# Optimization experiments

Hardware: AMD Instinct MI355X
Metric: run time of the kernel (lower is better)

The kernel has to match this reference:

```python
import jax, jax.numpy as jnp
import numpy as np

# Plane axes from generate_planes(); projection uses their inverses (permutation matrices).
_PLANES = np.array([[[1, 0, 0], [0, 1, 0], [0, 0, 1]],
                    [[1, 0, 0], [0, 0, 1], [0, 1, 0]],
                    [[0, 0, 1], [1, 0, 0], [0, 1, 0]]], dtype=np.float32)
_INV_PLANES = np.linalg.inv(_PLANES)  # [3,3,3]


def _grid_sample_2d(feat, grid):
    """Bilinear grid_sample, padding_mode='zeros', align_corners=False.
    feat: [C,H,W], grid: [M,2] with (x,y) in normalized coords. Returns [C,M]."""
    C, H, W = feat.shape
    x = ((grid[:, 0] + 1.0) * W - 1.0) * 0.5  # [M] pixel coords
    y = ((grid[:, 1] + 1.0) * H - 1.0) * 0.5
    x0 = jnp.floor(x)
    y0 = jnp.floor(y)
    wx = x - x0  # weight of right/bottom neighbor
    wy = y - y0
    x0i = x0.astype(jnp.int32)
    y0i = y0.astype(jnp.int32)
    x1i = x0i + 1
    y1i = y0i + 1

    def corner(xi, yi):
        valid = (xi >= 0) & (xi < W) & (yi >= 0) & (yi < H)
        xc = jnp.clip(xi, 0, W - 1)
        yc = jnp.clip(yi, 0, H - 1)
        v = feat[:, yc, xc]  # [C, M] gather
        return v * valid.astype(feat.dtype)

    v00 = corner(x0i, y0i)
    v10 = corner(x1i, y0i)
    v01 = corner(x0i, y1i)
    v11 = corner(x1i, y1i)
    out = (v00 * (1.0 - wx) * (1.0 - wy)
           + v10 * wx * (1.0 - wy)
           + v01 * (1.0 - wx) * wy
           + v11 * wx * wy)
    return out  # [C, M]


def setup_inputs() -> dict:
    key = jax.random.key(0)
    k1, k2, k3 = jax.random.split(key, 3)
    N, P, C, H, W, M = 4, 3, 32, 256, 256, 500000
    planes = jax.random.normal(k1, (N, P, C, H, W), dtype=jnp.float32)
    sample_coordinates = jax.random.uniform(k2, (N, M, 3), dtype=jnp.float32,
                                            minval=-1.0, maxval=1.0)
    sample_directions = jax.random.normal(k3, (N, M, 3), dtype=jnp.float32)
    return {"planes": planes, "sample_coordinates": sample_coordinates,
            "sample_directions": sample_directions}


def reference(planes, sample_coordinates, sample_directions):
    # ImportanceRenderer.run_model: project -> grid_sample per plane -> mean over planes.
    N, n_planes, C, H, W = planes.shape
    M = sample_coordinates.shape[1]
    inv = jnp.asarray(_INV_PLANES, dtype=sample_coordinates.dtype)  # [P,3,3]
    # torch.bmm(coords, inv_planes): [N,P,M,3] @ [P,3,3] -> take first 2 dims
    proj = jnp.einsum('nmi,pij->npmj', sample_coordinates, inv)[..., :2]  # [N,P,M,2]
    feats = planes.reshape(N * n_planes, C, H, W)
    grids = proj.reshape(N * n_planes, M, 2)
    sampled = jax.vmap(_grid_sample_2d)(feats, grids)  # [N*P, C, M]
    sampled = sampled.reshape(N, n_planes, C, M).transpose(0, 1, 3, 2)  # [N,P,M,C]
    return sampled.mean(axis=1)  # [N, M, C]
```

## Files before the change

kernel.cpp:

```cpp
#include <hip/hip_runtime.h>
#include <hip/hip_fp16.h>


constexpr int Cc = 32, Hh = 256, Ww = 256, Pp = 3, Nn = 4;
constexpr int HWPIX = Hh * Ww;
constexpr int NCO   = 4096;
constexpr int CB    = 2048;

__device__ inline unsigned spread3(unsigned x) {
    x &= 0x3FFu;
    x = (x | (x << 16)) & 0x030000FFu;
    x = (x | (x << 8))  & 0x0300F00Fu;
    x = (x | (x << 4))  & 0x030C30C3u;
    x = (x | (x << 2))  & 0x09249249u;
    return x;
}
__device__ inline unsigned coarse_key(float cx, float cy, float cz) {
    const int a = min(max((int)((cx + 1.0f) * 8.0f), 0), 15);
    const int b = min(max((int)((cy + 1.0f) * 8.0f), 0), 15);
    const int c = min(max((int)((cz + 1.0f) * 8.0f), 0), 15);
    return spread3((unsigned)a) | (spread3((unsigned)b) << 1) | (spread3((unsigned)c) << 2);
}

__global__ __launch_bounds__(256) void transpose_chw_hwc_h(
    const float* __restrict__ in, __half* __restrict__ out)
{
    __shared__ float lds[Cc * 257];
    const int slice = blockIdx.y;
    const int pix0  = blockIdx.x * 256;
    const int t     = threadIdx.x;

    const float* src = in + (size_t)slice * Cc * HWPIX + pix0 + t;
    #pragma unroll
    for (int c = 0; c < Cc; ++c)
        lds[c * 257 + t] = src[(size_t)c * HWPIX];
    __syncthreads();

    uint4* dst = reinterpret_cast<uint4*>(
        out + (size_t)slice * HWPIX * Cc + (size_t)pix0 * Cc);
    #pragma unroll
    for (int k = 0; k < 4; ++k) {
        const int idx = k * 256 + t;
        const int pix = idx >> 2;
        const int c0  = (idx & 3) * 8;
        unsigned r[4];
        #pragma unroll
        for (int j = 0; j < 4; ++j) {
            const __half h0 = __float2half(lds[(c0 + 2 * j + 0) * 257 + pix]);
            const __half h1 = __float2half(lds[(c0 + 2 * j + 1) * 257 + pix]);
            r[j] = (unsigned)__half_as_ushort(h0)
                 | ((unsigned)__half_as_ushort(h1) << 16);
        }
        dst[idx] = make_uint4(r[0], r[1], r[2], r[3]);
    }
}

__global__ __launch_bounds__(256) void block_hist(
    const float* __restrict__ coords, unsigned* __restrict__ bh, int M, int nb)
{
    __shared__ unsigned h[NCO];
    const int n = blockIdx.y, b = blockIdx.x, t = threadIdx.x;
    #pragma unroll
    for (int k = 0; k < NCO / 256; ++k) h[k * 256 + t] = 0u;
    __syncthreads();

    const int base = b * CB;
    for (int j = t; j < CB; j += 256) {
        const int m = base + j;
        if (m < M) {
            const float* cp = coords + ((size_t)n * M + m) * 3;
            atomicAdd(&h[coarse_key(cp[0], cp[1], cp[2])], 1u);
        }
    }
    __syncthreads();
    unsigned* dst = bh + ((size_t)n * nb + b) * NCO;
    #pragma unroll
    for (int k = 0; k < NCO / 256; ++k) dst[k * 256 + t] = h[k * 256 + t];
}

__global__ __launch_bounds__(256) void col_prefix(
    unsigned* __restrict__ bh, unsigned* __restrict__ tot, int nb)
{
    const int n = blockIdx.y;
    const int c = blockIdx.x * 256 + threadIdx.x;
    unsigned* p = bh + (size_t)n * nb * NCO + c;
    unsigned run = 0;
    for (int b = 0; b < nb; ++b) {
        const unsigned v = p[(size_t)b * NCO];
        p[(size_t)b * NCO] = run;
        run += v;
    }
    tot[n * NCO + c] = run;
}

__global__ __launch_bounds__(1024) void cell_scan(unsigned* __restrict__ tot)
{
    __shared__ unsigned lds[1024];
    unsigned* h = tot + (size_t)blockIdx.x * NCO;
    const int t = threadIdx.x;
    unsigned v[4];
    unsigned s = 0;
    #pragma unroll
    for (int i = 0; i < 4; ++i) { v[i] = h[t * 4 + i]; s += v[i]; }
    lds[t] = s;
    __syncthreads();
    for (int d = 1; d < 1024; d <<= 1) {
        const unsigned add = (t >= d) ? lds[t - d] : 0u;
        __syncthreads();
        lds[t] += add;
        __syncthreads();
    }
    unsigned base = (t > 0) ? lds[t - 1] : 0u;
    #pragma unroll
    for (int i = 0; i < 4; ++i) { const unsigned tmp = v[i]; h[t * 4 + i] = base; base += tmp; }
}

__global__ __launch_bounds__(256) void block_scatter(
    const float* __restrict__ coords, const unsigned* __restrict__ bh,
    const unsigned* __restrict__ cellbase, unsigned* __restrict__ idx,
    int M, int nb)
{
    __shared__ unsigned h[NCO];
    const int n = blockIdx.y, b = blockIdx.x, t = threadIdx.x;
    #pragma unroll
    for (int k = 0; k < NCO / 256; ++k) h[k * 256 + t] = 0u;
    __syncthreads();

    const unsigned* myrow = bh + ((size_t)n * nb + b) * NCO;
    const int base = b * CB;
    for (int j = t; j < CB; j += 256) {
        const int m = base + j;
        if (m < M) {
            const float* cp = coords + ((size_t)n * M + m) * 3;
            const unsigned k = coarse_key(cp[0], cp[1], cp[2]);
            const unsigned r = atomicAdd(&h[k], 1u);
            const unsigned slot = cellbase[n * NCO + k] + myrow[k] + r;
            idx[(size_t)n * M + slot] = (unsigned)m;
        }
    }
}

__global__ __launch_bounds__(256) void triplane_gather4h(
    const __half* __restrict__ tp, const unsigned* __restrict__ idx,
    const float* __restrict__ coords, float* __restrict__ out,
    int M, int gx, int nwg)
{
    int bid = blockIdx.x;
    {
        const int q = nwg >> 3, r = nwg & 7;
        const int xcd = bid & 7, i = bid >> 3;
        bid = (xcd < r ? xcd * (q + 1) : r * (q + 1) + (xcd - r) * q) + i;
    }
    const int n  = bid / gx;
    const int bx = bid - n * gx;
    const int gid  = bx * 256 + threadIdx.x;
    const int s    = gid >> 2;
    const int quad = gid & 3;
    if (s >= M) return;

    const int m = (int)idx[(size_t)n * M + s];
    const float* cp = coords + ((size_t)n * M + m) * 3;
    const float cx = cp[0], cy = cp[1], cz = cp[2];

    const uint4* addr[12];
    __half2 wh[12];

    #pragma unroll
    for (int p = 0; p < 3; ++p) {
        const float gxc = (p == 2) ? cz : cx;
        const float gyc = (p == 0) ? cy : ((p == 1) ? cz : cx);
        const float x = ((gxc + 1.0f) * 256.0f - 1.0f) * 0.5f;
        const float y = ((gyc + 1.0f) * 256.0f - 1.0f) * 0.5f;
        const float x0f = floorf(x), y0f = floorf(y);
        const float wx = x - x0f, wy = y - y0f;
        const int x0 = (int)x0f, y0 = (int)y0f;
        const int x1 = x0 + 1,   y1 = y0 + 1;
        const bool vx0 = (unsigned)x0 < 256u;
        const bool vx1 = (unsigned)x1 < 256u;
        const bool vy0 = (unsigned)y0 < 256u;
        const bool vy1 = (unsigned)y1 < 256u;
        const int cx0 = min(max(x0, 0), 255), cx1 = min(max(x1, 0), 255);
        const int cy0 = min(max(y0, 0), 255), cy1 = min(max(y1, 0), 255);

        const float w00 = ((vx0 && vy0) ? 1.f : 0.f) * (1.f - wx) * (1.f - wy);
        const float w10 = ((vx1 && vy0) ? 1.f : 0.f) * wx * (1.f - wy);
        const float w01 = ((vx0 && vy1) ? 1.f : 0.f) * (1.f - wx) * wy;
        const float w11 = ((vx1 && vy1) ? 1.f : 0.f) * wx * wy;
        wh[p * 4 + 0] = __float2half2_rn(w00);
        wh[p * 4 + 1] = __float2half2_rn(w10);
        wh[p * 4 + 2] = __float2half2_rn(w01);
        wh[p * 4 + 3] = __float2half2_rn(w11);

        const uint4* base = reinterpret_cast<const uint4*>(
            tp + (size_t)(n * 3 + p) * HWPIX * Cc);
        addr[p * 4 + 0] = base + (size_t)((cy0 << 8) + cx0) * 4 + quad;
        addr[p * 4 + 1] = base + (size_t)((cy0 << 8) + cx1) * 4 + quad;
        addr[p * 4 + 2] = base + (size_t)((cy1 << 8) + cx0) * 4 + quad;
        addr[p * 4 + 3] = base + (size_t)((cy1 << 8) + cx1) * 4 + quad;
    }

    uint4 rv[12];
    #pragma unroll
    for (int j = 0; j < 12; ++j) rv[j] = *addr[j];

    float accx[8];
    #pragma unroll
    for (int i = 0; i < 8; ++i) accx[i] = 0.f;

    #pragma unroll
    for (int p = 0; p < 3; ++p) {
        __half2 a0 = __float2half2_rn(0.f), a1 = a0, a2 = a0, a3 = a0;
        #pragma unroll
        for (int c = 0; c < 4; ++c) {
            const uint4 v = rv[p * 4 + c];
            const __half2 w = wh[p * 4 + c];
            a0 = __hfma2(*reinterpret_cast<const __half2*>(&v.x), w, a0);
            a1 = __hfma2(*reinterpret_cast<const __half2*>(&v.y), w, a1);
            a2 = __hfma2(*reinterpret_cast<const __half2*>(&v.z), w, a2);
            a3 = __hfma2(*reinterpret_cast<const __half2*>(&v.w), w, a3);
        }
        const float2 f0 = __half22float2(a0);
        const float2 f1 = __half22float2(a1);
        const float2 f2 = __half22float2(a2);
        const float2 f3 = __half22float2(a3);
        accx[0] += f0.x; accx[1] += f0.y;
        accx[2] += f1.x; accx[3] += f1.y;
        accx[4] += f2.x; accx[5] += f2.y;
        accx[6] += f3.x; accx[7] += f3.y;
    }

    constexpr float third = 1.0f / 3.0f;
    float4 o0, o1;
    o0.x = accx[0] * third; o0.y = accx[1] * third;
    o0.z = accx[2] * third; o0.w = accx[3] * third;
    o1.x = accx[4] * third; o1.y = accx[5] * third;
    o1.z = accx[6] * third; o1.w = accx[7] * third;

    float4* op = reinterpret_cast<float4*>(out + ((size_t)n * M + m) * Cc);
    op[quad * 2 + 0] = o0;
    op[quad * 2 + 1] = o1;
}

__global__ __launch_bounds__(256) void triplane_gather_hwc8h(
    const __half* __restrict__ tp, const float* __restrict__ coords,
    float* __restrict__ out, int M)
{
    const int gid   = blockIdx.x * 256 + threadIdx.x;
    const int m     = gid >> 3;
    const int chunk = gid & 7;
    const int n     = blockIdx.y;
    if (m >= M) return;

    const float* cp = coords + ((size_t)n * M + m) * 3;
    const float cx = cp[0], cy = cp[1], cz = cp[2];

    const uint2* addr[12];
    float w[12];

    #pragma unroll
    for (int p = 0; p < 3; ++p) {
        const float gxc = (p == 2) ? cz : cx;
        const float gyc = (p == 0) ? cy : ((p == 1) ? cz : cx);
        const float x = ((gxc + 1.0f) * 256.0f - 1.0f) * 0.5f;
        const float y = ((gyc + 1.0f) * 256.0f - 1.0f) * 0.5f;
        const float x0f = floorf(x), y0f = floorf(y);
        const float wx = x - x0f, wy = y - y0f;
        const int x0 = (int)x0f, y0 = (int)y0f;
        const int x1 = x0 + 1,   y1 = y0 + 1;
        const bool vx0 = (unsigned)x0 < 256u;
        const bool vx1 = (unsigned)x1 < 256u;
        const bool vy0 = (unsigned)y0 < 256u;
        const bool vy1 = (unsigned)y1 < 256u;
        const int cx0 = min(max(x0, 0), 255), cx1 = min(max(x1, 0), 255);
        const int cy0 = min(max(y0, 0), 255), cy1 = min(max(y1, 0), 255);

        w[p * 4 + 0] = ((vx0 && vy0) ? 1.f : 0.f) * (1.f - wx) * (1.f - wy);
        w[p * 4 + 1] = ((vx1 && vy0) ? 1.f : 0.f) * wx * (1.f - wy);
        w[p * 4 + 2] = ((vx0 && vy1) ? 1.f : 0.f) * (1.f - wx) * wy;
        w[p * 4 + 3] = ((vx1 && vy1) ? 1.f : 0.f) * wx * wy;

        const uint2* base = reinterpret_cast<const uint2*>(
            tp + (size_t)(n * 3 + p) * HWPIX * Cc);
        addr[p * 4 + 0] = base + (size_t)((cy0 << 8) + cx0) * 8 + chunk;
        addr[p * 4 + 1] = base + (size_t)((cy0 << 8) + cx1) * 8 + chunk;
        addr[p * 4 + 2] = base + (size_t)((cy1 << 8) + cx0) * 8 + chunk;
        addr[p * 4 + 3] = base + (size_t)((cy1 << 8) + cx1) * 8 + chunk;
    }

    uint2 rv[12];
    #pragma unroll
    for (int j = 0; j < 12; ++j) rv[j] = *addr[j];

    float4 acc = make_float4(0.f, 0.f, 0.f, 0.f);
    #pragma unroll
    for (int j = 0; j < 12; ++j) {
        const __half2 h0 = *reinterpret_cast<const __half2*>(&rv[j].x);
        const __half2 h1 = *reinterpret_cast<const __half2*>(&rv[j].y);
        const float2 f0 = __half22float2(h0);
        const float2 f1 = __half22float2(h1);
        acc.x += w[j] * f0.x;
        acc.y += w[j] * f0.y;
        acc.z += w[j] * f1.x;
        acc.w += w[j] * f1.y;
    }

    constexpr float third = 1.0f / 3.0f;
    acc.x *= third; acc.y *= third; acc.z *= third; acc.w *= third;

    float4* op = reinterpret_cast<float4*>(out + ((size_t)n * M + m) * Cc);
    op[chunk] = acc;
}

__global__ __launch_bounds__(256) void triplane_gather_chw(
    const float* __restrict__ planes, const float* __restrict__ coords,
    float* __restrict__ out, int M)
{
    const int m = blockIdx.x * 256 + threadIdx.x;
    const int n = blockIdx.y;
    if (m >= M) return;

    const float* cp = coords + ((size_t)n * M + m) * 3;
    const float cx = cp[0], cy = cp[1], cz = cp[2];

    int   off[3][4];
    float w[3][4];
    #pragma unroll
    for (int p = 0; p < 3; ++p) {
        const float gxc = (p == 2) ? cz : cx;
        const float gyc = (p == 0) ? cy : ((p == 1) ? cz : cx);
        const float x = ((gxc + 1.0f) * 256.0f - 1.0f) * 0.5f;
        const float y = ((gyc + 1.0f) * 256.0f - 1.0f) * 0.5f;
        const float x0f = floorf(x), y0f = floorf(y);
        const float wx = x - x0f, wy = y - y0f;
        const int x0 = (int)x0f, y0 = (int)y0f;
        const int x1 = x0 + 1,   y1 = y0 + 1;
        const bool vx0 = (unsigned)x0 < 256u, vx1 = (unsigned)x1 < 256u;
        const bool vy0 = (unsigned)y0 < 256u, vy1 = (unsigned)y1 < 256u;
        const int cx0 = min(max(x0, 0), 255), cx1 = min(max(x1, 0), 255);
        const int cy0 = min(max(y0, 0), 255), cy1 = min(max(y1, 0), 255);
        off[p][0] = (cy0 << 8) + cx0;  w[p][0] = ((vx0 && vy0) ? 1.f : 0.f) * (1.f - wx) * (1.f - wy);
        off[p][1] = (cy0 << 8) + cx1;  w[p][1] = ((vx1 && vy0) ? 1.f : 0.f) * wx * (1.f - wy);
        off[p][2] = (cy1 << 8) + cx0;  w[p][2] = ((vx0 && vy1) ? 1.f : 0.f) * (1.f - wx) * wy;
        off[p][3] = (cy1 << 8) + cx1;  w[p][3] = ((vx1 && vy1) ? 1.f : 0.f) * wx * wy;
    }

    float* op = out + ((size_t)n * M + m) * Cc;
    constexpr float third = 1.0f / 3.0f;
    for (int c = 0; c < Cc; ++c) {
        float a = 0.f;
        #pragma unroll
        for (int p = 0; p < 3; ++p) {
            const float* b = planes + ((size_t)(n * 3 + p) * Cc + c) * HWPIX;
            a += w[p][0] * b[off[p][0]] + w[p][1] * b[off[p][1]]
               + w[p][2] * b[off[p][2]] + w[p][3] * b[off[p][3]];
        }
        op[c] = a * third;
    }
}

extern "C" void kernel_launch(void* const* d_in, const int* in_sizes, int n_in,
                              void* d_out, int out_size, void* d_ws, size_t ws_size,
                              hipStream_t stream)
{
    const float* planes = (const float*)d_in[0];
    const float* coords = (const float*)d_in[1];
    float* out = (float*)d_out;

    const int M  = in_sizes[1] / (Nn * 3);
    const int nb = (M + CB - 1) / CB;

    auto align256 = [](size_t x) { return (x + 255) & ~(size_t)255; };
    const size_t tph_bytes = align256((size_t)Nn * Pp * HWPIX * Cc * sizeof(__half));
    const size_t idx_bytes = align256((size_t)Nn * M * sizeof(unsigned));
    const size_t bh_bytes  = align256((size_t)Nn * nb * NCO * sizeof(unsigned));
    const size_t tot_bytes = align256((size_t)Nn * NCO * sizeof(unsigned));

    if (ws_size >= tph_bytes + idx_bytes + bh_bytes + tot_bytes) {
        char* p = (char*)d_ws;
        __half*   tp  = (__half*)p;    p += tph_bytes;
        unsigned* idx = (unsigned*)p;  p += idx_bytes;
        unsigned* bh  = (unsigned*)p;  p += bh_bytes;
        unsigned* tot = (unsigned*)p;

        transpose_chw_hwc_h<<<dim3(HWPIX / 256, Nn * Pp), 256, 0, stream>>>(planes, tp);
        block_hist<<<dim3(nb, Nn), 256, 0, stream>>>(coords, bh, M, nb);
        col_prefix<<<dim3(NCO / 256, Nn), 256, 0, stream>>>(bh, tot, nb);
        cell_scan<<<Nn, 1024, 0, stream>>>(tot);
        block_scatter<<<dim3(nb, Nn), 256, 0, stream>>>(coords, bh, tot, idx, M, nb);

        const int gx  = (M * 4 + 255) / 256;
        const int nwg = Nn * gx;
        triplane_gather4h<<<nwg, 256, 0, stream>>>(tp, idx, coords, out, M, gx, nwg);
    } else if (ws_size >= tph_bytes) {
        __half* tp = (__half*)d_ws;
        transpose_chw_hwc_h<<<dim3(HWPIX / 256, Nn * Pp), 256, 0, stream>>>(planes, tp);
        const int gx = (M * 8 + 255) / 256;
        triplane_gather_hwc8h<<<dim3(gx, Nn), 256, 0, stream>>>(tp, coords, out, M);
    } else {
        const int gx = (M + 255) / 256;
        triplane_gather_chw<<<dim3(gx, Nn), 256, 0, stream>>>(planes, coords, out, M);
    }
}
```

Before: 284.2 us.

## Replace two-pass block histogram sort with capped global-atomic bin scatter

Replaces the block histogram, column prefix and block scatter counting sort with one pass that appends sample indices into fixed-capacity per-cell bins using global atomics. Overflow samples go to a tail list. A cell scan and a compaction kernel then build the dense ordering. The aim is to cut the number of passes over the coordinates and the large per-block histogram traffic. The cost is heavy global atomic contention, roughly 16 MB of extra bin storage, and an ordering within each cell that is no longer deterministic. The output stores also become nontemporal.

After: 285.0 us. Within noise of the previous version (+0.3%).

```diff
diff --git a/kernel.cpp b/kernel.cpp
--- a/kernel.cpp
+++ b/kernel.cpp
@@ -5,7 +5,9 @@
 constexpr int Cc = 32, Hh = 256, Ww = 256, Pp = 3, Nn = 4;
 constexpr int HWPIX = Hh * Ww;
 constexpr int NCO   = 4096;
-constexpr int CB    = 2048;
+constexpr int CAP   = 256;
+
+typedef float f32x4 __attribute__((ext_vector_type(4)));
 
 __device__ inline unsigned spread3(unsigned x) {
     x &= 0x3FFu;
@@ -55,53 +57,42 @@
     }
 }
 
-__global__ __launch_bounds__(256) void block_hist(
-    const float* __restrict__ coords, unsigned* __restrict__ bh, int M, int nb)
-{
-    __shared__ unsigned h[NCO];
-    const int n = blockIdx.y, b = blockIdx.x, t = threadIdx.x;
-    #pragma unroll
-    for (int k = 0; k < NCO / 256; ++k) h[k * 256 + t] = 0u;
-    __syncthreads();
-
-    const int base = b * CB;
-    for (int j = t; j < CB; j += 256) {
-        const int m = base + j;
-        if (m < M) {
-            const float* cp = coords + ((size_t)n * M + m) * 3;
-            atomicAdd(&h[coarse_key(cp[0], cp[1], cp[2])], 1u);
-        }
-    }
-    __syncthreads();
-    unsigned* dst = bh + ((size_t)n * nb + b) * NCO;
-    #pragma unroll
-    for (int k = 0; k < NCO / 256; ++k) dst[k * 256 + t] = h[k * 256 + t];
-}
-
-__global__ __launch_bounds__(256) void col_prefix(
-    unsigned* __restrict__ bh, unsigned* __restrict__ tot, int nb)
-{
+__global__ __launch_bounds__(256) void zero_u32(unsigned* __restrict__ p, int n)
+{
+    const int i = blockIdx.x * 256 + threadIdx.x;
+    if (i < n) p[i] = 0u;
+}
+
+__global__ __launch_bounds__(256) void bin_scatter(
+    const float* __restrict__ coords, unsigned* __restrict__ count,
+    unsigned* __restrict__ tailcnt, unsigned* __restrict__ bin,
+    unsigned* __restrict__ tail, int M)
+{
+    const int m = blockIdx.x * 256 + threadIdx.x;
     const int n = blockIdx.y;
-    const int c = blockIdx.x * 256 + threadIdx.x;
-    unsigned* p = bh + (size_t)n * nb * NCO + c;
-    unsigned run = 0;
-    for (int b = 0; b < nb; ++b) {
-        const unsigned v = p[(size_t)b * NCO];
-        p[(size_t)b * NCO] = run;
-        run += v;
-    }
-    tot[n * NCO + c] = run;
-}
-
-__global__ __launch_bounds__(1024) void cell_scan(unsigned* __restrict__ tot)
+    if (m >= M) return;
+    const float* cp = coords + ((size_t)n * M + m) * 3;
+    const unsigned k = coarse_key(cp[0], cp[1], cp[2]);
+    const unsigned r = atomicAdd(&count[n * NCO + k], 1u);
+    if (r < CAP) {
+        bin[(((size_t)n * NCO + k) << 8) + r] = (unsigned)m;
+    } else {
+        const unsigned t = atomicAdd(&tailcnt[n], 1u);
+        tail[(size_t)n * M + t] = (unsigned)m;
+    }
+}
+
+__global__ __launch_bounds__(1024) void cell_scan_base(
+    const unsigned* __restrict__ count, unsigned* __restrict__ base)
 {
     __shared__ unsigned lds[1024];
-    unsigned* h = tot + (size_t)blockIdx.x * NCO;
+    const unsigned* h = count + (size_t)blockIdx.x * NCO;
+    unsigned* o = base + (size_t)blockIdx.x * NCO;
     const int t = threadIdx.x;
     unsigned v[4];
     unsigned s = 0;
     #pragma unroll
-    for (int i = 0; i < 4; ++i) { v[i] = h[t * 4 + i]; s += v[i]; }
+    for (int i = 0; i < 4; ++i) { v[i] = min(h[t * 4 + i], (unsigned)CAP); s += v[i]; }
     lds[t] = s;
     __syncthreads();
     for (int d = 1; d < 1024; d <<= 1) {
@@ -110,34 +101,30 @@
         lds[t] += add;
         __syncthreads();
     }
-    unsigned base = (t > 0) ? lds[t - 1] : 0u;
-    #pragma unroll
-    for (int i = 0; i < 4; ++i) { const unsigned tmp = v[i]; h[t * 4 + i] = base; base += tmp; }
-}
-
-__global__ __launch_bounds__(256) void block_scatter(
-    const float* __restrict__ coords, const unsigned* __restrict__ bh,
-    const unsigned* __restrict__ cellbase, unsigned* __restrict__ idx,
-    int M, int nb)
-{
-    __shared__ unsigned h[NCO];
-    const int n = blockIdx.y, b = blockIdx.x, t = threadIdx.x;
-    #pragma unroll
-    for (int k = 0; k < NCO / 256; ++k) h[k * 256 + t] = 0u;
-    __syncthreads();
-
-    const unsigned* myrow = bh + ((size_t)n * nb + b) * NCO;
-    const int base = b * CB;
-    for (int j = t; j < CB; j += 256) {
-        const int m = base + j;
-        if (m < M) {
-            const float* cp = coords + ((size_t)n * M + m) * 3;
-            const unsigned k = coarse_key(cp[0], cp[1], cp[2]);
-            const unsigned r = atomicAdd(&h[k], 1u);
-            const unsigned slot = cellbase[n * NCO + k] + myrow[k] + r;
-            idx[(size_t)n * M + slot] = (unsigned)m;
-        }
-    }
+    unsigned b = (t > 0) ? lds[t - 1] : 0u;
+    #pragma unroll
+    for (int i = 0; i < 4; ++i) { const unsigned tmp = v[i]; o[t * 4 + i] = b; b += tmp; }
+}
+
+__global__ __launch_bounds__(256) void compact_cells(
+    const unsigned* __restrict__ count, const unsigned* __restrict__ base,
+    const unsigned* __restrict__ bin, unsigned* __restrict__ dense, int M)
+{
+    const int n = blockIdx.y, cell = blockIdx.x, t = threadIdx.x;
+    const unsigned c = min(count[n * NCO + cell], (unsigned)CAP);
+    if ((unsigned)t < c)
+        dense[(size_t)n * M + base[n * NCO + cell] + t] =
+            bin[(((size_t)n * NCO + cell) << 8) + t];
+}
+
+__global__ __launch_bounds__(256) void tail_copy(
+    const unsigned* __restrict__ tailcnt, const unsigned* __restrict__ tail,
+    unsigned* __restrict__ dense, int M)
+{
+    const int n = blockIdx.x;
+    const unsigned tc = tailcnt[n];
+    for (unsigned t = threadIdx.x; t < tc; t += 256)
+        dense[(size_t)n * M + (M - tc) + t] = tail[(size_t)n * M + t];
 }
 
 __global__ __launch_bounds__(256) void triplane_gather4h(
@@ -230,15 +217,15 @@
     }
 
     constexpr float third = 1.0f / 3.0f;
-    float4 o0, o1;
+    f32x4 o0, o1;
     o0.x = accx[0] * third; o0.y = accx[1] * third;
     o0.z = accx[2] * third; o0.w = accx[3] * third;
     o1.x = accx[4] * third; o1.y = accx[5] * third;
     o1.z = accx[6] * third; o1.w = accx[7] * third;
 
-    float4* op = reinterpret_cast<float4*>(out + ((size_t)n * M + m) * Cc);
-    op[quad * 2 + 0] = o0;
-    op[quad * 2 + 1] = o1;
+    f32x4* op = reinterpret_cast<f32x4*>(out + ((size_t)n * M + m) * Cc);
+    __builtin_nontemporal_store(o0, op + quad * 2 + 0);
+    __builtin_nontemporal_store(o1, op + quad * 2 + 1);
 }
 
 __global__ __launch_bounds__(256) void triplane_gather_hwc8h(
@@ -366,31 +353,42 @@
     const float* coords = (const float*)d_in[1];
     float* out = (float*)d_out;
 
-    const int M  = in_sizes[1] / (Nn * 3);
-    const int nb = (M + CB - 1) / CB;
+    const int M = in_sizes[1] / (Nn * 3);
 
     auto align256 = [](size_t x) { return (x + 255) & ~(size_t)255; };
-    const size_t tph_bytes = align256((size_t)Nn * Pp * HWPIX * Cc * sizeof(__half));
-    const size_t idx_bytes = align256((size_t)Nn * M * sizeof(unsigned));
-    const size_t bh_bytes  = align256((size_t)Nn * nb * NCO * sizeof(unsigned));
-    const size_t tot_bytes = align256((size_t)Nn * NCO * sizeof(unsigned));
-
-    if (ws_size >= tph_bytes + idx_bytes + bh_bytes + tot_bytes) {
+    const size_t tph_bytes   = align256((size_t)Nn * Pp * HWPIX * Cc * sizeof(__half));
+    const size_t bin_bytes   = align256((size_t)Nn * NCO * CAP * sizeof(unsigned));
+    const size_t dense_bytes = align256((size_t)Nn * M * sizeof(unsigned));
+    const size_t tail_bytes  = align256((size_t)Nn * M * sizeof(unsigned));
+    const size_t cnt_bytes   = align256((size_t)Nn * NCO * sizeof(unsigned));
+    const size_t base_bytes  = align256((size_t)Nn * NCO * sizeof(unsigned));
+    const size_t tc_bytes    = align256((size_t)Nn * sizeof(unsigned));
+
+    const size_t need = tph_bytes + bin_bytes + dense_bytes + tail_bytes +
+                        cnt_bytes + base_bytes + tc_bytes;
+
+    if (ws_size >= need) {
         char* p = (char*)d_ws;
-        __half*   tp  = (__half*)p;    p += tph_bytes;
-        unsigned* idx = (unsigned*)p;  p += idx_bytes;
-        unsigned* bh  = (unsigned*)p;  p += bh_bytes;
-        unsigned* tot = (unsigned*)p;
+        __half*   tp      = (__half*)p;   p += tph_bytes;
+        unsigned* bin     = (unsigned*)p; p += bin_bytes;
+        unsigned* dense   = (unsigned*)p; p += dense_bytes;
+        unsigned* tail    = (unsigned*)p; p += tail_bytes;
+        unsigned* count   = (unsigned*)p; p += cnt_bytes;
+        unsigned* base    = (unsigned*)p; p += base_bytes;
+        unsigned* tailcnt = (unsigned*)p;
 
         transpose_chw_hwc_h<<<dim3(HWPIX / 256, Nn * Pp), 256, 0, stream>>>(planes, tp);
-        block_hist<<<dim3(nb, Nn), 256, 0, stream>>>(coords, bh, M, nb);
-        col_prefix<<<dim3(NCO / 256, Nn), 256, 0, stream>>>(bh, tot, nb);
-        cell_scan<<<Nn, 1024, 0, stream>>>(tot);
-        block_scatter<<<dim3(nb, Nn), 256, 0, stream>>>(coords, bh, tot, idx, M, nb);
+        zero_u32<<<(Nn * NCO + 255) / 256, 256, 0, stream>>>(count, Nn * NCO);
+        zero_u32<<<1, 256, 0, stream>>>(tailcnt, Nn);
+        bin_scatter<<<dim3((M + 255) / 256, Nn), 256, 0, stream>>>(
+            coords, count, tailcnt, bin, tail, M);
+        cell_scan_base<<<Nn, 1024, 0, stream>>>(count, base);
+        compact_cells<<<dim3(NCO, Nn), 256, 0, stream>>>(count, base, bin, dense, M);
+        tail_copy<<<Nn, 256, 0, stream>>>(tailcnt, tail, dense, M);
 
         const int gx  = (M * 4 + 255) / 256;
         const int nwg = Nn * gx;
-        triplane_gather4h<<<nwg, 256, 0, stream>>>(tp, idx, coords, out, M, gx, nwg);
+        triplane_gather4h<<<nwg, 256, 0, stream>>>(tp, dense, coords, out, M, gx, nwg);
     } else if (ws_size >= tph_bytes) {
         __half* tp = (__half*)d_ws;
         transpose_chw_hwc_h<<<dim3(HWPIX / 256, Nn * Pp), 256, 0, stream>>>(planes, tp);
```

## Fuse transpose and counting sort into one cooperative kernel with grid syncs

Applied to the files above, without the earlier changes.

Replaces the separate transpose, per-block histogram, column prefix, cell scan and scatter kernels with a single cooperative kernel. It does the fp16 HWC transpose, then uses global atomics for per-cell counts, a small scan, and a scatter, with grid-wide syncs between phases. This removes several launches and the per-block histogram traffic. In exchange it relies on contended global atomics, grid sync overhead and a fixed 1024-block grid. Output stores in the gather kernel also become nontemporal.

Result: slower. 635.4 us (+123.6%).

```diff
diff --git a/kernel.cpp b/kernel.cpp
--- a/kernel.cpp
+++ b/kernel.cpp
@@ -1,11 +1,19 @@
 #include <hip/hip_runtime.h>
 #include <hip/hip_fp16.h>
+#include <hip/hip_cooperative_groups.h>
+
+namespace cg = cooperative_groups;
 
 
 constexpr int Cc = 32, Hh = 256, Ww = 256, Pp = 3, Nn = 4;
 constexpr int HWPIX = Hh * Ww;
 constexpr int NCO   = 4096;
-constexpr int CB    = 2048;
+
+constexpr int GRID = 1024, BLK = 256;
+constexpr int TT   = GRID * BLK;
+constexpr int NIT  = 2;
+
+typedef float f32x4 __attribute__((ext_vector_type(4)));
 
 __device__ inline unsigned spread3(unsigned x) {
     x &= 0x3FFu;
@@ -22,120 +30,103 @@
     return spread3((unsigned)a) | (spread3((unsigned)b) << 1) | (spread3((unsigned)c) << 2);
 }
 
-__global__ __launch_bounds__(256) void transpose_chw_hwc_h(
-    const float* __restrict__ in, __half* __restrict__ out)
-{
-    __shared__ float lds[Cc * 257];
-    const int slice = blockIdx.y;
-    const int pix0  = blockIdx.x * 256;
-    const int t     = threadIdx.x;
-
-    const float* src = in + (size_t)slice * Cc * HWPIX + pix0 + t;
-    #pragma unroll
-    for (int c = 0; c < Cc; ++c)
-        lds[c * 257 + t] = src[(size_t)c * HWPIX];
-    __syncthreads();
-
-    uint4* dst = reinterpret_cast<uint4*>(
-        out + (size_t)slice * HWPIX * Cc + (size_t)pix0 * Cc);
-    #pragma unroll
-    for (int k = 0; k < 4; ++k) {
-        const int idx = k * 256 + t;
-        const int pix = idx >> 2;
-        const int c0  = (idx & 3) * 8;
-        unsigned r[4];
-        #pragma unroll
-        for (int j = 0; j < 4; ++j) {
-            const __half h0 = __float2half(lds[(c0 + 2 * j + 0) * 257 + pix]);
-            const __half h1 = __float2half(lds[(c0 + 2 * j + 1) * 257 + pix]);
-            r[j] = (unsigned)__half_as_ushort(h0)
-                 | ((unsigned)__half_as_ushort(h1) << 16);
-        }
-        dst[idx] = make_uint4(r[0], r[1], r[2], r[3]);
-    }
-}
-
-__global__ __launch_bounds__(256) void block_hist(
-    const float* __restrict__ coords, unsigned* __restrict__ bh, int M, int nb)
-{
-    __shared__ unsigned h[NCO];
-    const int n = blockIdx.y, b = blockIdx.x, t = threadIdx.x;
-    #pragma unroll
-    for (int k = 0; k < NCO / 256; ++k) h[k * 256 + t] = 0u;
-    __syncthreads();
-
-    const int base = b * CB;
-    for (int j = t; j < CB; j += 256) {
-        const int m = base + j;
-        if (m < M) {
-            const float* cp = coords + ((size_t)n * M + m) * 3;
-            atomicAdd(&h[coarse_key(cp[0], cp[1], cp[2])], 1u);
-        }
-    }
-    __syncthreads();
-    unsigned* dst = bh + ((size_t)n * nb + b) * NCO;
-    #pragma unroll
-    for (int k = 0; k < NCO / 256; ++k) dst[k * 256 + t] = h[k * 256 + t];
-}
-
-__global__ __launch_bounds__(256) void col_prefix(
-    unsigned* __restrict__ bh, unsigned* __restrict__ tot, int nb)
-{
-    const int n = blockIdx.y;
-    const int c = blockIdx.x * 256 + threadIdx.x;
-    unsigned* p = bh + (size_t)n * nb * NCO + c;
-    unsigned run = 0;
-    for (int b = 0; b < nb; ++b) {
-        const unsigned v = p[(size_t)b * NCO];
-        p[(size_t)b * NCO] = run;
-        run += v;
-    }
-    tot[n * NCO + c] = run;
-}
-
-__global__ __launch_bounds__(1024) void cell_scan(unsigned* __restrict__ tot)
-{
-    __shared__ unsigned lds[1024];
-    unsigned* h = tot + (size_t)blockIdx.x * NCO;
-    const int t = threadIdx.x;
-    unsigned v[4];
-    unsigned s = 0;
-    #pragma unroll
-    for (int i = 0; i < 4; ++i) { v[i] = h[t * 4 + i]; s += v[i]; }
-    lds[t] = s;
-    __syncthreads();
-    for (int d = 1; d < 1024; d <<= 1) {
-        const unsigned add = (t >= d) ? lds[t - d] : 0u;
+__global__ __launch_bounds__(256) void fused_prep(
+    const float* __restrict__ planes, const float* __restrict__ coords,
+    __half* __restrict__ tp, unsigned* __restrict__ cnt,
+    unsigned* __restrict__ idx, int M)
+{
+    __shared__ float lds[Cc * 129];
+    const int tid = blockIdx.x * BLK + threadIdx.x;
+    const int t   = threadIdx.x;
+
+    for (int i = tid; i < Nn * NCO; i += TT) cnt[i] = 0u;
+
+    const int ntiles = Nn * Pp * (HWPIX / 128);
+    for (int tile = blockIdx.x; tile < ntiles; tile += GRID) {
+        const int slice = tile / (HWPIX / 128);
+        const int pix0  = (tile - slice * (HWPIX / 128)) * 128;
         __syncthreads();
-        lds[t] += add;
+        const int p = t & 127, half = t >> 7;
+        const float* src = planes + (size_t)slice * Cc * HWPIX + pix0 + p;
+        #pragma unroll
+        for (int c16 = 0; c16 < 16; ++c16) {
+            const int c = half * 16 + c16;
+            lds[c * 129 + p] = src[(size_t)c * HWPIX];
+        }
         __syncthreads();
-    }
-    unsigned base = (t > 0) ? lds[t - 1] : 0u;
-    #pragma unroll
-    for (int i = 0; i < 4; ++i) { const unsigned tmp = v[i]; h[t * 4 + i] = base; base += tmp; }
-}
-
-__global__ __launch_bounds__(256) void block_scatter(
-    const float* __restrict__ coords, const unsigned* __restrict__ bh,
-    const unsigned* __restrict__ cellbase, unsigned* __restrict__ idx,
-    int M, int nb)
-{
-    __shared__ unsigned h[NCO];
-    const int n = blockIdx.y, b = blockIdx.x, t = threadIdx.x;
-    #pragma unroll
-    for (int k = 0; k < NCO / 256; ++k) h[k * 256 + t] = 0u;
-    __syncthreads();
-
-    const unsigned* myrow = bh + ((size_t)n * nb + b) * NCO;
-    const int base = b * CB;
-    for (int j = t; j < CB; j += 256) {
-        const int m = base + j;
-        if (m < M) {
-            const float* cp = coords + ((size_t)n * M + m) * 3;
-            const unsigned k = coarse_key(cp[0], cp[1], cp[2]);
-            const unsigned r = atomicAdd(&h[k], 1u);
-            const unsigned slot = cellbase[n * NCO + k] + myrow[k] + r;
-            idx[(size_t)n * M + slot] = (unsigned)m;
+        uint4* dst = reinterpret_cast<uint4*>(
+            tp + (size_t)slice * HWPIX * Cc + (size_t)pix0 * Cc);
+        #pragma unroll
+        for (int k = 0; k < 2; ++k) {
+            const int id  = k * 256 + t;
+            const int pix = id >> 2;
+            const int c0  = (id & 3) * 8;
+            unsigned r[4];
+            #pragma unroll
+            for (int j = 0; j < 4; ++j) {
+                const __half h0 = __float2half(lds[(c0 + 2 * j + 0) * 129 + pix]);
+                const __half h1 = __float2half(lds[(c0 + 2 * j + 1) * 129 + pix]);
+                r[j] = (unsigned)__half_as_ushort(h0)
+                     | ((unsigned)__half_as_ushort(h1) << 16);
+            }
+            dst[id] = make_uint4(r[0], r[1], r[2], r[3]);
+        }
+    }
+
+    cg::this_grid().sync();
+
+    unsigned kp[Nn][NIT];
+    #pragma unroll
+    for (int n = 0; n < Nn; ++n) {
+        #pragma unroll
+        for (int it = 0; it < NIT; ++it) {
+            const int m = tid + it * TT;
+            unsigned v = 0xFFFFFFFFu;
+            if (m < M) {
+                const float* cp = coords + ((size_t)n * M + m) * 3;
+                const unsigned k = coarse_key(cp[0], cp[1], cp[2]);
+                const unsigned pos = atomicAdd(&cnt[n * NCO + k], 1u);
+                v = k | (pos << 12);
+            }
+            kp[n][it] = v;
+        }
+    }
+
+    cg::this_grid().sync();
+
+    if (blockIdx.x < Nn) {
+        unsigned* h = cnt + blockIdx.x * NCO;
+        unsigned* slds = reinterpret_cast<unsigned*>(lds);
+        unsigned v[16];
+        unsigned s = 0;
+        #pragma unroll
+        for (int i = 0; i < 16; ++i) { v[i] = h[t * 16 + i]; s += v[i]; }
+        slds[t] = s;
+        __syncthreads();
+        for (int d = 1; d < 256; d <<= 1) {
+            const unsigned add = (t >= d) ? slds[t - d] : 0u;
+            __syncthreads();
+            slds[t] += add;
+            __syncthreads();
+        }
+        unsigned b = (t > 0) ? slds[t - 1] : 0u;
+        #pragma unroll
+        for (int i = 0; i < 16; ++i) { const unsigned tmp = v[i]; h[t * 16 + i] = b; b += tmp; }
+    }
+
+    cg::this_grid().sync();
+
+    #pragma unroll
+    for (int n = 0; n < Nn; ++n) {
+        #pragma unroll
+        for (int it = 0; it < NIT; ++it) {
+            const int m = tid + it * TT;
+            if (m < M) {
+                const unsigned v   = kp[n][it];
+                const unsigned k   = v & 0xFFFu;
+                const unsigned pos = v >> 12;
+                idx[(size_t)n * M + cnt[n * NCO + k] + pos] = (unsigned)m;
+            }
         }
     }
 }
@@ -230,15 +221,48 @@
     }
 
     constexpr float third = 1.0f / 3.0f;
-    float4 o0, o1;
+    f32x4 o0, o1;
     o0.x = accx[0] * third; o0.y = accx[1] * third;
     o0.z = accx[2] * third; o0.w = accx[3] * third;
     o1.x = accx[4] * third; o1.y = accx[5] * third;
     o1.z = accx[6] * third; o1.w = accx[7] * third;
 
-    float4* op = reinterpret_cast<float4*>(out + ((size_t)n * M + m) * Cc);
-    op[quad * 2 + 0] = o0;
-    op[quad * 2 + 1] = o1;
+    f32x4* op = reinterpret_cast<f32x4*>(out + ((size_t)n * M + m) * Cc);
+    __builtin_nontemporal_store(o0, op + quad * 2 + 0);
+    __builtin_nontemporal_store(o1, op + quad * 2 + 1);
+}
+
+__global__ __launch_bounds__(256) void transpose_chw_hwc_h(
+    const float* __restrict__ in, __half* __restrict__ out)
+{
+    __shared__ float lds[Cc * 257];
+    const int slice = blockIdx.y;
+    const int pix0  = blockIdx.x * 256;
+    const int t     = threadIdx.x;
+
+    const float* src = in + (size_t)slice * Cc * HWPIX + pix0 + t;
+    #pragma unroll
+    for (int c = 0; c < Cc; ++c)
+        lds[c * 257 + t] = src[(size_t)c * HWPIX];
+    __syncthreads();
+
+    uint4* dst = reinterpret_cast<uint4*>(
+        out + (size_t)slice * HWPIX * Cc + (size_t)pix0 * Cc);
+    #pragma unroll
+    for (int k = 0; k < 4; ++k) {
+        const int idx = k * 256 + t;
+        const int pix = idx >> 2;
+        const int c0  = (idx & 3) * 8;
+        unsigned r[4];
+        #pragma unroll
+        for (int j = 0; j < 4; ++j) {
+            const __half h0 = __float2half(lds[(c0 + 2 * j + 0) * 257 + pix]);
+            const __half h1 = __float2half(lds[(c0 + 2 * j + 1) * 257 + pix]);
+            r[j] = (unsigned)__half_as_ushort(h0)
+                 | ((unsigned)__half_as_ushort(h1) << 16);
+        }
+        dst[idx] = make_uint4(r[0], r[1], r[2], r[3]);
+    }
 }
 
 __global__ __launch_bounds__(256) void triplane_gather_hwc8h(
@@ -366,38 +390,41 @@
     const float* coords = (const float*)d_in[1];
     float* out = (float*)d_out;
 
-    const int M  = in_sizes[1] / (Nn * 3);
-    const int nb = (M + CB - 1) / CB;
+    const int M = in_sizes[1] / (Nn * 3);
 
     auto align256 = [](size_t x) { return (x + 255) & ~(size_t)255; };
     const size_t tph_bytes = align256((size_t)Nn * Pp * HWPIX * Cc * sizeof(__half));
     const size_t idx_bytes = align256((size_t)Nn * M * sizeof(unsigned));
-    const size_t bh_bytes  = align256((size_t)Nn * nb * NCO * sizeof(unsigned));
-    const size_t tot_bytes = align256((size_t)Nn * NCO * sizeof(unsigned));
-
-    if (ws_size >= tph_bytes + idx_bytes + bh_bytes + tot_bytes) {
+    const size_t cnt_bytes = align256((size_t)Nn * NCO * sizeof(unsigned));
+
+    bool done = false;
+    if (ws_size >= tph_bytes + idx_bytes + cnt_bytes && M <= NIT * TT) {
         char* p = (char*)d_ws;
         __half*   tp  = (__half*)p;    p += tph_bytes;
         unsigned* idx = (unsigned*)p;  p += idx_bytes;
-        unsigned* bh  = (unsigned*)p;  p += bh_bytes;
-        unsigned* tot = (unsigned*)p;
-
-        transpose_chw_hwc_h<<<dim3(HWPIX / 256, Nn * Pp), 256, 0, stream>>>(planes, tp);
-        block_hist<<<dim3(nb, Nn), 256, 0, stream>>>(coords, bh, M, nb);
-        col_prefix<<<dim3(NCO / 256, Nn), 256, 0, stream>>>(bh, tot, nb);
-        cell_scan<<<Nn, 1024, 0, stream>>>(tot);
-        block_scatter<<<dim3(nb, Nn), 256, 0, stream>>>(coords, bh, tot, idx, M, nb);
-
-        const int gx  = (M * 4 + 255) / 256;
-        const int nwg = Nn * gx;
-        triplane_gather4h<<<nwg, 256, 0, stream>>>(tp, idx, coords, out, M, gx, nwg);
-    } else if (ws_size >= tph_bytes) {
-        __half* tp = (__half*)d_ws;
-        transpose_chw_hwc_h<<<dim3(HWPIX / 256, Nn * Pp), 256, 0, stream>>>(planes, tp);
-        const int gx = (M * 8 + 255) / 256;
-        triplane_gather_hwc8h<<<dim3(gx, Nn), 256, 0, stream>>>(tp, coords, out, M);
-    } else {
-        const int gx = (M + 255) / 256;
-        triplane_gather_chw<<<dim3(gx, Nn), 256, 0, stream>>>(planes, coords, out, M);
-    }
-}
+        unsigned* cnt = (unsigned*)p;
+
+        void* args[] = { (void*)&planes, (void*)&coords, (void*)&tp,
+                         (void*)&cnt, (void*)&idx, (void*)&M };
+        const hipError_t e = hipLaunchCooperativeKernel(
+            (const void*)fused_prep, dim3(GRID), dim3(BLK), args, 0, stream);
+        if (e == hipSuccess) {
+            const int gx  = (M * 4 + 255) / 256;
+            const int nwg = Nn * gx;
+            triplane_gather4h<<<nwg, 256, 0, stream>>>(tp, idx, coords, out, M, gx, nwg);
+            done = true;
+        }
+    }
+
+    if (!done) {
+        if (ws_size >= tph_bytes) {
+            __half* tp = (__half*)d_ws;
+            transpose_chw_hwc_h<<<dim3(HWPIX / 256, Nn * Pp), 256, 0, stream>>>(planes, tp);
+            const int gx = (M * 8 + 255) / 256;
+            triplane_gather_hwc8h<<<dim3(gx, Nn), 256, 0, stream>>>(tp, coords, out, M);
+        } else {
+            const int gx = (M + 255) / 256;
+            triplane_gather_chw<<<dim3(gx, Nn), 256, 0, stream>>>(planes, coords, out, M);
+        }
+    }
+}
```
